# Kernel optimization log

Hardware: AMD Instinct MI355X
Metric: run time of the kernel (lower is better)

Reference implementation:

```python
import jax, jax.numpy as jnp
import numpy as np

B, C, H, W = 8, 512, 32, 32
N_HEADS = 4
D_K = C // N_HEADS  # 128


def setup_inputs() -> dict:
    key = jax.random.key(0)
    k1, k2, k3, k4, k5 = jax.random.split(key, 5)
    x = jax.random.normal(k1, (B, C, H, W), dtype=jnp.float32)
    # projection: Linear(in_ch, n_heads*d_k*3)
    Wp = jax.random.normal(k2, (C, N_HEADS * D_K * 3), dtype=jnp.float32) * (C ** -0.5)
    bp = jax.random.normal(k3, (N_HEADS * D_K * 3,), dtype=jnp.float32) * 0.01
    # output: Linear(n_heads*d_k, in_ch)
    Wo = jax.random.normal(k4, (N_HEADS * D_K, C), dtype=jnp.float32) * ((N_HEADS * D_K) ** -0.5)
    bo = jax.random.normal(k5, (C,), dtype=jnp.float32) * 0.01
    return {"x": x, "Wp": Wp, "bp": bp, "Wo": Wo, "bo": bo}


def reference(x, Wp, bp, Wo, bo):
    b, c, h, w = x.shape
    scale = D_K ** -0.5
    # [B, C, H, W] -> [B, N, C], N = H*W
    xs = x.reshape(b, c, h * w).transpose(0, 2, 1)
    qkv = (xs @ Wp + bp).reshape(b, h * w, N_HEADS, 3 * D_K)
    q, k, v = jnp.split(qkv, 3, axis=-1)  # each [B, N, H, D]
    attn = jnp.einsum('bihd,bjhd->bijh', q, k) * scale
    attn = jax.nn.softmax(attn, axis=2)  # softmax over j (keys)
    out = jnp.einsum('bijh,bjhd->bihd', attn, v)
    out = out.reshape(b, h * w, N_HEADS * D_K)
    out = out @ Wo + bo
    out = out + xs  # residual (note: GroupNorm is unused in the original forward)
    return out.transpose(0, 2, 1).reshape(b, c, h, w)
```

## Files before the change

### kernel.cpp

```cpp
#include <hip/hip_runtime.h>

#define NB 8
#define NC 512
#define NTOK 1024
#define NHEADS 4
#define DKH 128

typedef unsigned short u16;
typedef __attribute__((ext_vector_type(8))) short bf16x8;
typedef __attribute__((ext_vector_type(4))) float f32x4;

__device__ inline u16 f2b(float f) {
    union { float f; unsigned u; } v; v.f = f;
    unsigned r = v.u + 0x7fffu + ((v.u >> 16) & 1u);
    return (u16)(r >> 16);
}

__device__ __forceinline__ void gll16(const u16* g, u16* l) {
    __builtin_amdgcn_global_load_lds((const __attribute__((address_space(1))) unsigned*)g,
                                     (__attribute__((address_space(3))) unsigned*)l, 16, 0, 0);
}

__global__ __launch_bounds__(256) void prep(const float* __restrict__ x, const float* __restrict__ Wp,
                                            const float* __restrict__ Wo,
                                            u16* __restrict__ xsb, u16* __restrict__ WpT, u16* __restrict__ WoT)
{
    __shared__ float tile[32][33];
    const int z = blockIdx.z;
    const float* src; u16* dst; int R, Cc;
    if (z == 0)      { src = Wp; dst = WpT; R = 512; Cc = 1536; }
    else if (z == 1) { if (blockIdx.x >= 16) return; src = Wo; dst = WoT; R = 512; Cc = 512; }
    else             { if (blockIdx.x >= 32) return;
                       src = x + (long)(z-2)*NC*NTOK; dst = xsb + (long)(z-2)*NTOK*NC; R = NC; Cc = NTOK; }
    int c0 = blockIdx.x * 32, r0 = blockIdx.y * 32;
    int tx = threadIdx.x, ty = threadIdx.y;
    #pragma unroll
    for (int k = 0; k < 4; ++k)
        tile[ty + 8*k][tx] = src[(long)(r0 + ty + 8*k) * Cc + c0 + tx];
    __syncthreads();
    #pragma unroll
    for (int k = 0; k < 4; ++k)
        dst[(long)(c0 + ty + 8*k) * R + r0 + tx] = f2b(tile[tx][ty + 8*k]);
}

__global__ __launch_bounds__(512, 2) void gemm_qkv(const u16* __restrict__ WpT, const u16* __restrict__ xsb,
                                                   const float* __restrict__ bp,
                                                   u16* __restrict__ qg, u16* __restrict__ kg, u16* __restrict__ vg)
{
    __shared__ union SmU {
        struct { u16 As[2][256][64]; u16 Bs[2][256][64]; } s;
        u16 Os[8][64][72];
    } sm;
    const int tid = threadIdx.x;
    const int raw = blockIdx.x;
    const int L = (raw & 7) * 24 + (raw >> 3);
    const int mb = L % 6, nb = L / 6;
    const int m0 = mb * 256;
    const int n0 = nb * 256;
    const int w = tid >> 6, lane = tid & 63, quad = lane >> 4, lc = lane & 15;
    const int mo = (w & 1) * 128, no = (w >> 1) * 64;
    const int sw8 = (((lane & 7) ^ (lane >> 3)) << 3);
    const int xs = lc & 7;
    const int srow = (lane >> 3);

    f32x4 acc[8][4] = {};

    #pragma unroll
    for (int p = 0; p < 4; ++p) {
        int row = w*32 + p*8 + srow;
        gll16(&WpT[(long)(m0 + row) * NC + 0 + sw8], &sm.s.As[0][w*32 + p*8][0]);
        gll16(&xsb[(long)(n0 + row) * NC + 0 + sw8], &sm.s.Bs[0][w*32 + p*8][0]);
    }

    for (int t = 0; t < 8; ++t) {
        if (t < 7) {
            const long kk = (long)(t + 1) * 64;
            const int nbuf = (t + 1) & 1;
            #pragma unroll
            for (int p = 0; p < 4; ++p) {
                int row = w*32 + p*8 + srow;
                gll16(&WpT[(long)(m0 + row) * NC + kk + sw8], &sm.s.As[nbuf][w*32 + p*8][0]);
                gll16(&xsb[(long)(n0 + row) * NC + kk + sw8], &sm.s.Bs[nbuf][w*32 + p*8][0]);
            }
            asm volatile("s_waitcnt vmcnt(8)" ::: "memory");
        } else {
            asm volatile("s_waitcnt vmcnt(0)" ::: "memory");
        }
        __builtin_amdgcn_s_barrier();
        __builtin_amdgcn_sched_barrier(0);

        const int cb = t & 1;
        #pragma unroll
        for (int ks = 0; ks < 2; ++ks) {
            bf16x8 af[8], bfr[4];
            #pragma unroll
            for (int mt = 0; mt < 8; ++mt)
                af[mt] = *(const bf16x8*)&sm.s.As[cb][mo + mt*16 + lc][((ks*4 + quad) ^ xs) << 3];
            #pragma unroll
            for (int nt = 0; nt < 4; ++nt)
                bfr[nt] = *(const bf16x8*)&sm.s.Bs[cb][no + nt*16 + lc][((ks*4 + quad) ^ xs) << 3];
            __builtin_amdgcn_s_setprio(1);
            #pragma unroll
            for (int mt = 0; mt < 8; ++mt)
                #pragma unroll
                for (int nt = 0; nt < 4; ++nt)
                    acc[mt][nt] = __builtin_amdgcn_mfma_f32_16x16x32_bf16(af[mt], bfr[nt], acc[mt][nt], 0, 0, 0);
            __builtin_amdgcn_s_setprio(0);
        }
        __builtin_amdgcn_s_barrier();
    }

    const int bb = n0 >> 10;
    const int nblk = n0 & 1023;
    const int pb = (m0 + mo) >> 7;
    const int h = pb / 3;
    const int sel = pb % 3;
    const long bhbase = (long)(bb * NHEADS + h);

    #pragma unroll
    for (int mh = 0; mh < 2; ++mh) {
        const int d0 = mh * 64;
        #pragma unroll
        for (int mt4 = 0; mt4 < 4; ++mt4) {
            int mt = mh*4 + mt4;
            int cq0 = m0 + mo + mt*16 + quad*4;
            float b0 = bp[cq0+0], b1 = bp[cq0+1], b2 = bp[cq0+2], b3 = bp[cq0+3];
            #pragma unroll
            for (int nt = 0; nt < 4; ++nt) {
                f32x4 a = acc[mt][nt];
                int nl = nt*16 + lc;
                int ml = mt4*16 + quad*4;
                u16 e0 = f2b(a[0]+b0), e1 = f2b(a[1]+b1), e2 = f2b(a[2]+b2), e3 = f2b(a[3]+b3);
                if (sel == 2) {
                    sm.Os[w][ml+0][nl] = e0; sm.Os[w][ml+1][nl] = e1;
                    sm.Os[w][ml+2][nl] = e2; sm.Os[w][ml+3][nl] = e3;
                } else {
                    sm.Os[w][nl][ml+0] = e0; sm.Os[w][nl][ml+1] = e1;
                    sm.Os[w][nl][ml+2] = e2; sm.Os[w][nl][ml+3] = e3;
                }
            }
        }
        __builtin_amdgcn_sched_barrier(0);

        if (sel == 2) {
            #pragma unroll
            for (int pass = 0; pass < 8; ++pass) {
                int ml  = pass*8 + srow;
                int nl0 = (lane & 7) * 8;
                bf16x8 vv = *(const bf16x8*)&sm.Os[w][ml][nl0];
                *(bf16x8*)&vg[((bhbase*DKH + d0 + ml) << 10) + nblk + no + sw8] = vv;
            }
        } else if (sel == 1) {
            #pragma unroll
            for (int pass = 0; pass < 8; ++pass) {
                int nl  = pass*8 + srow;
                int ml0 = (lane & 7) * 8;
                bf16x8 vv = *(const bf16x8*)&sm.Os[w][nl][ml0];
                *(bf16x8*)&kg[((bhbase*NTOK + nblk + no + nl) << 7) + d0 + sw8] = vv;
            }
        } else {
            #pragma unroll
            for (int pass = 0; pass < 8; ++pass) {
                int nl  = pass*8 + srow;
                int ml0 = (lane & 7) * 8;
                bf16x8 vv = *(const bf16x8*)&sm.Os[w][nl][ml0];
                *(bf16x8*)&qg[((bhbase*NTOK + nblk + no + nl) << 7) + d0 + ml0] = vv;
            }
        }
        __builtin_amdgcn_sched_barrier(0);
    }
}

__global__ __launch_bounds__(512) void attn(const u16* __restrict__ qg, const u16* __restrict__ kg,
                                            const u16* __restrict__ vtg, u16* __restrict__ ho)
{
    __shared__ union {
        struct { u16 Ks[2][64*128]; u16 Vt[2][128*64]; u16 Ps[8][32][40]; } m;
        struct { float Om[4][2][32][68]; float Lm[2][4][32]; } g;
    } sm;
    const int tid = threadIdx.x;
    const int w = tid >> 6, lane = tid & 63, quad = lane >> 4, lc = lane & 15;
    const int iw = w & 3, jw = w >> 2;
    const int id = blockIdx.x;
    const int xcd = id & 7, rest = id >> 3, sub = rest & 3, bx = rest >> 2;
    const int pr = xcd + sub*8;
    const int b = pr >> 2, h = pr & 3;
    const int i0 = bx*128 + iw*32;
    const long bh = (long)(b * NHEADS + h) << 17;
    const u16* qb = qg + bh;
    const u16* kb = kg + bh;
    const u16* vb = vtg + bh;
    const float SL2E = 0.08838834764831845f * 1.4426950408889634f;

    bf16x8 qf[2][4];
    #pragma unroll
    for (int it = 0; it < 2; ++it)
        #pragma unroll
        for (int ks = 0; ks < 4; ++ks)
            qf[it][ks] = *(const bf16x8*)&qb[(long)(i0 + it*16 + lc) * DKH + ks*32 + quad*8];

    f32x4 o[2][8] = {};
    float lsum[2] = {0.f, 0.f};
    const int xs = lc & 7;

    #pragma unroll
    for (int p = 0; p < 2; ++p) {
        int ck = (w*2 + p)*64 + lane;
        gll16(&kb[(long)ck * 8], &sm.m.Ks[0][(w*2 + p)*512]);
        gll16(&vb[(((long)(ck >> 3)) << 10) + (ck & 7)*8], &sm.m.Vt[0][(w*2 + p)*512]);
    }

    for (int t = 0; t < 16; ++t) {
        __syncthreads();
        if (t < 15) {
            long jo = (long)(t+1) * 64;
            #pragma unroll
            for (int p = 0; p < 2; ++p) {
                int ck = (w*2 + p)*64 + lane;
                gll16(&kb[jo*128 + (long)ck*8], &sm.m.Ks[(t+1)&1][(w*2 + p)*512]);
                gll16(&vb[(((long)(ck >> 3)) << 10) + jo + (ck & 7)*8], &sm.m.Vt[(t+1)&1][(w*2 + p)*512]);
            }
        }
        const u16* K = sm.m.Ks[t&1];
        const u16* V = sm.m.Vt[t&1];

        f32x4 s[2][2] = {};
        #pragma unroll
        for (int ks = 0; ks < 4; ++ks)
            #pragma unroll
            for (int jt = 0; jt < 2; ++jt) {
                bf16x8 kf = *(const bf16x8*)&K[(jw*32 + jt*16 + lc)*128 + (((ks*4 + quad) ^ xs) << 3)];
                s[0][jt] = __builtin_amdgcn_mfma_f32_16x16x32_bf16(kf, qf[0][ks], s[0][jt], 0, 0, 0);
                s[1][jt] = __builtin_amdgcn_mfma_f32_16x16x32_bf16(kf, qf[1][ks], s[1][jt], 0, 0, 0);
            }

        #pragma unroll
        for (int it = 0; it < 2; ++it)
            #pragma unroll
            for (int jt = 0; jt < 2; ++jt) {
                float p0 = __builtin_amdgcn_exp2f(s[it][jt][0] * SL2E);
                float p1 = __builtin_amdgcn_exp2f(s[it][jt][1] * SL2E);
                float p2 = __builtin_amdgcn_exp2f(s[it][jt][2] * SL2E);
                float p3 = __builtin_amdgcn_exp2f(s[it][jt][3] * SL2E);
                lsum[it] += (p0 + p1) + (p2 + p3);
                ushort4 pk;
                pk.x = f2b(p0); pk.y = f2b(p1); pk.z = f2b(p2); pk.w = f2b(p3);
                *(ushort4*)&sm.m.Ps[w][it*16 + lc][jt*16 + quad*4] = pk;
            }
        __builtin_amdgcn_sched_barrier(0);

        bf16x8 pf0 = *(const bf16x8*)&sm.m.Ps[w][lc]     [quad*8];
        bf16x8 pf1 = *(const bf16x8*)&sm.m.Ps[w][16 + lc][quad*8];
        #pragma unroll
        for (int dt = 0; dt < 8; ++dt) {
            bf16x8 vf = *(const bf16x8*)&V[(dt*16 + lc)*64 + (((jw*4 + quad) ^ xs) << 3)];
            o[0][dt] = __builtin_amdgcn_mfma_f32_16x16x32_bf16(vf, pf0, o[0][dt], 0, 0, 0);
            o[1][dt] = __builtin_amdgcn_mfma_f32_16x16x32_bf16(vf, pf1, o[1][dt], 0, 0, 0);
        }
    }

    #pragma unroll
    for (int it = 0; it < 2; ++it) {
        lsum[it] += __shfl_xor(lsum[it], 16);
        lsum[it] += __shfl_xor(lsum[it], 32);
    }

    __syncthreads();
    #pragma unroll
    for (int it = 0; it < 2; ++it) {
        if (jw == 0) {
            #pragma unroll
            for (int d4 = 0; d4 < 4; ++d4)
                *(f32x4*)&sm.g.Om[iw][1][it*16 + lc][d4*16 + quad*4] = o[it][4 + d4];
        } else {
            #pragma unroll
            for (int d4 = 0; d4 < 4; ++d4)
                *(f32x4*)&sm.g.Om[iw][0][it*16 + lc][d4*16 + quad*4] = o[it][d4];
        }
        if (quad == 0) sm.g.Lm[jw][iw][it*16 + lc] = lsum[it];
    }
    __syncthreads();
    #pragma unroll
    for (int it = 0; it < 2; ++it) {
        float lt = lsum[it] + sm.g.Lm[1 - jw][iw][it*16 + lc];
        float inv = 1.0f / lt;
        long rowbase = (long)(b*NTOK + i0 + it*16 + lc) * NC + h*DKH + jw*64;
        if (jw == 0) {
            #pragma unroll
            for (int d4 = 0; d4 < 4; ++d4) {
                f32x4 part = *(const f32x4*)&sm.g.Om[iw][0][it*16 + lc][d4*16 + quad*4];
                f32x4 tot = o[it][d4] + part;
                ushort4 pk;
                pk.x = f2b(tot[0] * inv); pk.y = f2b(tot[1] * inv);
                pk.z = f2b(tot[2] * inv); pk.w = f2b(tot[3] * inv);
                *(ushort4*)&ho[rowbase + d4*16 + quad*4] = pk;
            }
        } else {
            #pragma unroll
            for (int d4 = 0; d4 < 4; ++d4) {
                f32x4 part = *(const f32x4*)&sm.g.Om[iw][1][it*16 + lc][d4*16 + quad*4];
                f32x4 tot = o[it][4 + d4] + part;
                ushort4 pk;
                pk.x = f2b(tot[0] * inv); pk.y = f2b(tot[1] * inv);
                pk.z = f2b(tot[2] * inv); pk.w = f2b(tot[3] * inv);
                *(ushort4*)&ho[rowbase + d4*16 + quad*4] = pk;
            }
        }
    }
}

__global__ __launch_bounds__(256) void gemm_out(const u16* __restrict__ WoT, const u16* __restrict__ ho,
                                                const float* __restrict__ bo, const float* __restrict__ xin,
                                                float* __restrict__ dout)
{
    __shared__ struct { u16 As[128][64]; u16 Bs[64][64]; } sm;
    const int tid = threadIdx.x;
    const int m0 = blockIdx.x * 128;
    const int n0 = blockIdx.y * 64;
    const int w = tid >> 6, lane = tid & 63, quad = lane >> 4, lc = lane & 15;
    const int mo = (w & 1) * 64, no = (w >> 1) * 32;
    const int sw8 = (((lane & 7) ^ (lane >> 3)) << 3);
    const int xs = lc & 7;

    f32x4 acc[4][2] = {};

    for (int k0 = 0; k0 < NC; k0 += 64) {
        __syncthreads();
        #pragma unroll
        for (int p = 0; p < 4; ++p) {
            int row = w*32 + p*8 + (lane >> 3);
            gll16(&WoT[(long)(m0 + row) * NC + k0 + sw8], &sm.As[w*32 + p*8][0]);
        }
        #pragma unroll
        for (int p = 0; p < 2; ++p) {
            int row = w*16 + p*8 + (lane >> 3);
            gll16(&ho[(long)(n0 + row) * NC + k0 + sw8], &sm.Bs[w*16 + p*8][0]);
        }
        __syncthreads();
        #pragma unroll
        for (int ks = 0; ks < 2; ++ks) {
            bf16x8 af[4], bfr[2];
            #pragma unroll
            for (int t = 0; t < 4; ++t)
                af[t] = *(const bf16x8*)&sm.As[mo + t*16 + lc][((ks*4 + quad) ^ xs) << 3];
            #pragma unroll
            for (int t = 0; t < 2; ++t)
                bfr[t] = *(const bf16x8*)&sm.Bs[no + t*16 + lc][((ks*4 + quad) ^ xs) << 3];
            #pragma unroll
            for (int mt = 0; mt < 4; ++mt)
                #pragma unroll
                for (int nt = 0; nt < 2; ++nt)
                    acc[mt][nt] = __builtin_amdgcn_mfma_f32_16x16x32_bf16(af[mt], bfr[nt], acc[mt][nt], 0, 0, 0);
        }
    }

    const int bb = n0 >> 10;
    #pragma unroll
    for (int mt = 0; mt < 4; ++mt) {
        int cc0 = m0 + mo + mt*16 + quad*4;
        float b0 = bo[cc0+0], b1 = bo[cc0+1], b2 = bo[cc0+2], b3 = bo[cc0+3];
        #pragma unroll
        for (int nt = 0; nt < 2; ++nt) {
            int nl = (n0 + no + nt*16 + lc) & (NTOK - 1);
            f32x4 a = acc[mt][nt];
            long ix = ((long)(bb*NC + cc0) << 10) + nl;
            dout[ix]             = a[0] + b0 + xin[ix];
            dout[ix + (1 << 10)] = a[1] + b1 + xin[ix + (1 << 10)];
            dout[ix + (2 << 10)] = a[2] + b2 + xin[ix + (2 << 10)];
            dout[ix + (3 << 10)] = a[3] + b3 + xin[ix + (3 << 10)];
        }
    }
}

extern "C" void kernel_launch(void* const* d_in, const int* in_sizes, int n_in,
                              void* d_out, int out_size, void* d_ws, size_t ws_size,
                              hipStream_t stream)
{
    (void)in_sizes; (void)n_in; (void)out_size; (void)ws_size;
    const float* x  = (const float*)d_in[0];
    const float* Wp = (const float*)d_in[1];
    const float* bp = (const float*)d_in[2];
    const float* Wo = (const float*)d_in[3];
    const float* bo = (const float*)d_in[4];
    float* out = (float*)d_out;

    u16* ws  = (u16*)d_ws;
    u16* xsb = ws;
    u16* WpT = xsb + (long)NB * NTOK * NC;
    u16* WoT = WpT + 1536L * 512;
    u16* qg  = WoT + 512L * 512;
    u16* kg  = qg + (long)NB * NHEADS * NTOK * DKH;
    u16* vtg = kg + (long)NB * NHEADS * NTOK * DKH;
    u16* ho  = vtg + (long)NB * NHEADS * NTOK * DKH;

    prep<<<dim3(48, 16, 10), dim3(32, 8), 0, stream>>>(x, Wp, Wo, xsb, WpT, WoT);
    gemm_qkv<<<dim3(192), 512, 0, stream>>>(WpT, xsb, bp, qg, kg, vtg);
    attn<<<dim3(256), 512, 0, stream>>>(qg, kg, vtg, ho);
    gemm_out<<<dim3(NC/128, (NB*NTOK)/64), 256, 0, stream>>>(WoT, ho, bo, x, out);
}
```

Baseline: 139.3 us.

## Fuse all four stages into one cooperative persistent kernel with grid syncs

Replaces the four separate launches (prep transpose, QKV GEMM, attention, output GEMM) with one cooperative kernel of 256 blocks. Grid-wide syncs separate the stages, and shared memory is a union across stages. The aim is to remove launch gaps and tail effects between kernels. In exchange, the output GEMM and prep work are reshaped to fit a fixed 256-block grid, the QKV stage uses only 192 blocks, and grid.sync adds its own overhead.

```diff
diff --git a/kernel.cpp b/kernel.cpp
--- a/kernel.cpp
+++ b/kernel.cpp
@@ -1,4 +1,7 @@
 #include <hip/hip_runtime.h>
+#include <hip/hip_cooperative_groups.h>
+
+namespace cg = cooperative_groups;
 
 #define NB 8
 #define NC 512
@@ -21,353 +24,345 @@
                                      (__attribute__((address_space(3))) unsigned*)l, 16, 0, 0);
 }
 
-__global__ __launch_bounds__(256) void prep(const float* __restrict__ x, const float* __restrict__ Wp,
-                                            const float* __restrict__ Wo,
-                                            u16* __restrict__ xsb, u16* __restrict__ WpT, u16* __restrict__ WoT)
+__global__ __launch_bounds__(512, 2) void fused(const float* __restrict__ x, const float* __restrict__ Wp,
+                                                const float* __restrict__ bp, const float* __restrict__ Wo,
+                                                const float* __restrict__ bo, float* __restrict__ dout,
+                                                u16* __restrict__ xsb, u16* __restrict__ WpT, u16* __restrict__ WoT,
+                                                u16* __restrict__ qg, u16* __restrict__ kg, u16* __restrict__ vtg,
+                                                u16* __restrict__ ho)
 {
-    __shared__ float tile[32][33];
-    const int z = blockIdx.z;
-    const float* src; u16* dst; int R, Cc;
-    if (z == 0)      { src = Wp; dst = WpT; R = 512; Cc = 1536; }
-    else if (z == 1) { if (blockIdx.x >= 16) return; src = Wo; dst = WoT; R = 512; Cc = 512; }
-    else             { if (blockIdx.x >= 32) return;
-                       src = x + (long)(z-2)*NC*NTOK; dst = xsb + (long)(z-2)*NTOK*NC; R = NC; Cc = NTOK; }
-    int c0 = blockIdx.x * 32, r0 = blockIdx.y * 32;
-    int tx = threadIdx.x, ty = threadIdx.y;
-    #pragma unroll
-    for (int k = 0; k < 4; ++k)
-        tile[ty + 8*k][tx] = src[(long)(r0 + ty + 8*k) * Cc + c0 + tx];
-    __syncthreads();
-    #pragma unroll
-    for (int k = 0; k < 4; ++k)
-        dst[(long)(c0 + ty + 8*k) * R + r0 + tx] = f2b(tile[tx][ty + 8*k]);
-}
-
-__global__ __launch_bounds__(512, 2) void gemm_qkv(const u16* __restrict__ WpT, const u16* __restrict__ xsb,
-                                                   const float* __restrict__ bp,
-                                                   u16* __restrict__ qg, u16* __restrict__ kg, u16* __restrict__ vg)
-{
-    __shared__ union SmU {
-        struct { u16 As[2][256][64]; u16 Bs[2][256][64]; } s;
-        u16 Os[8][64][72];
+    __shared__ union FS {
+        float pt[2][32][33];
+        union { struct { u16 As[2][256][64]; u16 Bs[2][256][64]; } s;
+                u16 Os[8][64][72]; } q;
+        union { struct { u16 Ks[2][8192]; u16 Vt[2][8192]; u16 Ps[8][32][40]; } m;
+                struct { float Om[4][2][32][68]; float Lm[2][4][32]; } g; } a;
+        struct { u16 As[128][64]; u16 Bs[128][64]; } o;
     } sm;
+
+    cg::grid_group grid = cg::this_grid();
     const int tid = threadIdx.x;
-    const int raw = blockIdx.x;
-    const int L = (raw & 7) * 24 + (raw >> 3);
-    const int mb = L % 6, nb = L / 6;
-    const int m0 = mb * 256;
-    const int n0 = nb * 256;
+    const int bid = blockIdx.x;
     const int w = tid >> 6, lane = tid & 63, quad = lane >> 4, lc = lane & 15;
-    const int mo = (w & 1) * 128, no = (w >> 1) * 64;
     const int sw8 = (((lane & 7) ^ (lane >> 3)) << 3);
     const int xs = lc & 7;
-    const int srow = (lane >> 3);
-
-    f32x4 acc[8][4] = {};
-
-    #pragma unroll
-    for (int p = 0; p < 4; ++p) {
-        int row = w*32 + p*8 + srow;
-        gll16(&WpT[(long)(m0 + row) * NC + 0 + sw8], &sm.s.As[0][w*32 + p*8][0]);
-        gll16(&xsb[(long)(n0 + row) * NC + 0 + sw8], &sm.s.Bs[0][w*32 + p*8][0]);
+    const int srow = lane >> 3;
+
+    {
+        const int half = tid >> 8, t256 = tid & 255;
+        const int tx = t256 & 31, ty = t256 >> 5;
+        for (int j = bid*2 + half; j < 5120; j += 512) {
+            const float* src; u16* dst; int R, Cc, bx, by;
+            if (j < 768)       { src = Wp; dst = WpT; R = 512; Cc = 1536; bx = j % 48; by = j / 48; }
+            else if (j < 1024) { int q2 = j - 768; src = Wo; dst = WoT; R = 512; Cc = 512; bx = q2 & 15; by = q2 >> 4; }
+            else               { int q2 = j - 1024; int z = q2 >> 9; int r = q2 & 511;
+                                 src = x + (long)z*NC*NTOK; dst = xsb + (long)z*NTOK*NC;
+                                 R = NC; Cc = NTOK; bx = r & 31; by = r >> 5; }
+            int c0 = bx*32, r0 = by*32;
+            #pragma unroll
+            for (int k = 0; k < 4; ++k)
+                sm.pt[half][ty + 8*k][tx] = src[(long)(r0 + ty + 8*k)*Cc + c0 + tx];
+            __syncthreads();
+            #pragma unroll
+            for (int k = 0; k < 4; ++k)
+                dst[(long)(c0 + ty + 8*k)*R + r0 + tx] = f2b(sm.pt[half][tx][ty + 8*k]);
+            __syncthreads();
+        }
     }
-
-    for (int t = 0; t < 8; ++t) {
-        if (t < 7) {
-            const long kk = (long)(t + 1) * 64;
-            const int nbuf = (t + 1) & 1;
-            #pragma unroll
-            for (int p = 0; p < 4; ++p) {
-                int row = w*32 + p*8 + srow;
-                gll16(&WpT[(long)(m0 + row) * NC + kk + sw8], &sm.s.As[nbuf][w*32 + p*8][0]);
-                gll16(&xsb[(long)(n0 + row) * NC + kk + sw8], &sm.s.Bs[nbuf][w*32 + p*8][0]);
-            }
-            asm volatile("s_waitcnt vmcnt(8)" ::: "memory");
-        } else {
-            asm volatile("s_waitcnt vmcnt(0)" ::: "memory");
-        }
-        __builtin_amdgcn_s_barrier();
-        __builtin_amdgcn_sched_barrier(0);
-
-        const int cb = t & 1;
-        #pragma unroll
-        for (int ks = 0; ks < 2; ++ks) {
-            bf16x8 af[8], bfr[4];
-            #pragma unroll
-            for (int mt = 0; mt < 8; ++mt)
-                af[mt] = *(const bf16x8*)&sm.s.As[cb][mo + mt*16 + lc][((ks*4 + quad) ^ xs) << 3];
-            #pragma unroll
-            for (int nt = 0; nt < 4; ++nt)
-                bfr[nt] = *(const bf16x8*)&sm.s.Bs[cb][no + nt*16 + lc][((ks*4 + quad) ^ xs) << 3];
-            __builtin_amdgcn_s_setprio(1);
-            #pragma unroll
-            for (int mt = 0; mt < 8; ++mt)
+    grid.sync();
+
+    if (bid < 192) {
+        const int L = (bid & 7) * 24 + (bid >> 3);
+        const int mb = L % 6, nb = L / 6;
+        const int m0 = mb * 256, n0 = nb * 256;
+        const int mo = (w & 1) * 128, no = (w >> 1) * 64;
+
+        f32x4 acc[8][4] = {};
+
+        #pragma unroll
+        for (int p = 0; p < 4; ++p) {
+            int row = w*32 + p*8 + srow;
+            gll16(&WpT[(long)(m0 + row) * NC + 0 + sw8], &sm.q.s.As[0][w*32 + p*8][0]);
+            gll16(&xsb[(long)(n0 + row) * NC + 0 + sw8], &sm.q.s.Bs[0][w*32 + p*8][0]);
+        }
+
+        for (int t = 0; t < 8; ++t) {
+            if (t < 7) {
+                const long kk = (long)(t + 1) * 64;
+                const int nbuf = (t + 1) & 1;
+                #pragma unroll
+                for (int p = 0; p < 4; ++p) {
+                    int row = w*32 + p*8 + srow;
+                    gll16(&WpT[(long)(m0 + row) * NC + kk + sw8], &sm.q.s.As[nbuf][w*32 + p*8][0]);
+                    gll16(&xsb[(long)(n0 + row) * NC + kk + sw8], &sm.q.s.Bs[nbuf][w*32 + p*8][0]);
+                }
+                asm volatile("s_waitcnt vmcnt(8)" ::: "memory");
+            } else {
+                asm volatile("s_waitcnt vmcnt(0)" ::: "memory");
+            }
+            __builtin_amdgcn_s_barrier();
+            __builtin_amdgcn_sched_barrier(0);
+
+            const int cb = t & 1;
+            #pragma unroll
+            for (int ks = 0; ks < 2; ++ks) {
+                bf16x8 af[8], bfr[4];
+                #pragma unroll
+                for (int mt = 0; mt < 8; ++mt)
+                    af[mt] = *(const bf16x8*)&sm.q.s.As[cb][mo + mt*16 + lc][((ks*4 + quad) ^ xs) << 3];
                 #pragma unroll
                 for (int nt = 0; nt < 4; ++nt)
-                    acc[mt][nt] = __builtin_amdgcn_mfma_f32_16x16x32_bf16(af[mt], bfr[nt], acc[mt][nt], 0, 0, 0);
-            __builtin_amdgcn_s_setprio(0);
-        }
-        __builtin_amdgcn_s_barrier();
+                    bfr[nt] = *(const bf16x8*)&sm.q.s.Bs[cb][no + nt*16 + lc][((ks*4 + quad) ^ xs) << 3];
+                __builtin_amdgcn_s_setprio(1);
+                #pragma unroll
+                for (int mt = 0; mt < 8; ++mt)
+                    #pragma unroll
+                    for (int nt = 0; nt < 4; ++nt)
+                        acc[mt][nt] = __builtin_amdgcn_mfma_f32_16x16x32_bf16(af[mt], bfr[nt], acc[mt][nt], 0, 0, 0);
+                __builtin_amdgcn_s_setprio(0);
+            }
+            __builtin_amdgcn_s_barrier();
+        }
+
+        const int bb = n0 >> 10;
+        const int nblk = n0 & 1023;
+        const int pb = (m0 + mo) >> 7;
+        const int h = pb / 3;
+        const int sel = pb % 3;
+        const long bhbase = (long)(bb * NHEADS + h);
+
+        #pragma unroll
+        for (int mh = 0; mh < 2; ++mh) {
+            const int d0 = mh * 64;
+            #pragma unroll
+            for (int mt4 = 0; mt4 < 4; ++mt4) {
+                int mt = mh*4 + mt4;
+                int cq0 = m0 + mo + mt*16 + quad*4;
+                float b0 = bp[cq0+0], b1 = bp[cq0+1], b2 = bp[cq0+2], b3 = bp[cq0+3];
+                #pragma unroll
+                for (int nt = 0; nt < 4; ++nt) {
+                    f32x4 aa = acc[mt][nt];
+                    int nl = nt*16 + lc;
+                    int ml = mt4*16 + quad*4;
+                    u16 e0 = f2b(aa[0]+b0), e1 = f2b(aa[1]+b1), e2 = f2b(aa[2]+b2), e3 = f2b(aa[3]+b3);
+                    if (sel == 2) {
+                        sm.q.Os[w][ml+0][nl] = e0; sm.q.Os[w][ml+1][nl] = e1;
+                        sm.q.Os[w][ml+2][nl] = e2; sm.q.Os[w][ml+3][nl] = e3;
+                    } else {
+                        sm.q.Os[w][nl][ml+0] = e0; sm.q.Os[w][nl][ml+1] = e1;
+                        sm.q.Os[w][nl][ml+2] = e2; sm.q.Os[w][nl][ml+3] = e3;
+                    }
+                }
+            }
+            __builtin_amdgcn_sched_barrier(0);
+
+            if (sel == 2) {
+                #pragma unroll
+                for (int pass = 0; pass < 8; ++pass) {
+                    int ml  = pass*8 + srow;
+                    int nl0 = (lane & 7) * 8;
+                    bf16x8 vv = *(const bf16x8*)&sm.q.Os[w][ml][nl0];
+                    *(bf16x8*)&vtg[((bhbase*DKH + d0 + ml) << 10) + nblk + no + sw8] = vv;
+                }
+            } else if (sel == 1) {
+                #pragma unroll
+                for (int pass = 0; pass < 8; ++pass) {
+                    int nl  = pass*8 + srow;
+                    int ml0 = (lane & 7) * 8;
+                    bf16x8 vv = *(const bf16x8*)&sm.q.Os[w][nl][ml0];
+                    *(bf16x8*)&kg[((bhbase*NTOK + nblk + no + nl) << 7) + d0 + sw8] = vv;
+                }
+            } else {
+                #pragma unroll
+                for (int pass = 0; pass < 8; ++pass) {
+                    int nl  = pass*8 + srow;
+                    int ml0 = (lane & 7) * 8;
+                    bf16x8 vv = *(const bf16x8*)&sm.q.Os[w][nl][ml0];
+                    *(bf16x8*)&qg[((bhbase*NTOK + nblk + no + nl) << 7) + d0 + ml0] = vv;
+                }
+            }
+            __builtin_amdgcn_sched_barrier(0);
+        }
     }
-
-    const int bb = n0 >> 10;
-    const int nblk = n0 & 1023;
-    const int pb = (m0 + mo) >> 7;
-    const int h = pb / 3;
-    const int sel = pb % 3;
-    const long bhbase = (long)(bb * NHEADS + h);
-
-    #pragma unroll
-    for (int mh = 0; mh < 2; ++mh) {
-        const int d0 = mh * 64;
-        #pragma unroll
-        for (int mt4 = 0; mt4 < 4; ++mt4) {
-            int mt = mh*4 + mt4;
-            int cq0 = m0 + mo + mt*16 + quad*4;
-            float b0 = bp[cq0+0], b1 = bp[cq0+1], b2 = bp[cq0+2], b3 = bp[cq0+3];
-            #pragma unroll
-            for (int nt = 0; nt < 4; ++nt) {
-                f32x4 a = acc[mt][nt];
-                int nl = nt*16 + lc;
-                int ml = mt4*16 + quad*4;
-                u16 e0 = f2b(a[0]+b0), e1 = f2b(a[1]+b1), e2 = f2b(a[2]+b2), e3 = f2b(a[3]+b3);
-                if (sel == 2) {
-                    sm.Os[w][ml+0][nl] = e0; sm.Os[w][ml+1][nl] = e1;
-                    sm.Os[w][ml+2][nl] = e2; sm.Os[w][ml+3][nl] = e3;
-                } else {
-                    sm.Os[w][nl][ml+0] = e0; sm.Os[w][nl][ml+1] = e1;
-                    sm.Os[w][nl][ml+2] = e2; sm.Os[w][nl][ml+3] = e3;
-                }
-            }
-        }
-        __builtin_amdgcn_sched_barrier(0);
-
-        if (sel == 2) {
-            #pragma unroll
-            for (int pass = 0; pass < 8; ++pass) {
-                int ml  = pass*8 + srow;
-                int nl0 = (lane & 7) * 8;
-                bf16x8 vv = *(const bf16x8*)&sm.Os[w][ml][nl0];
-                *(bf16x8*)&vg[((bhbase*DKH + d0 + ml) << 10) + nblk + no + sw8] = vv;
-            }
-        } else if (sel == 1) {
-            #pragma unroll
-            for (int pass = 0; pass < 8; ++pass) {
-                int nl  = pass*8 + srow;
-                int ml0 = (lane & 7) * 8;
-                bf16x8 vv = *(const bf16x8*)&sm.Os[w][nl][ml0];
-                *(bf16x8*)&kg[((bhbase*NTOK + nblk + no + nl) << 7) + d0 + sw8] = vv;
-            }
-        } else {
-            #pragma unroll
-            for (int pass = 0; pass < 8; ++pass) {
-                int nl  = pass*8 + srow;
-                int ml0 = (lane & 7) * 8;
-                bf16x8 vv = *(const bf16x8*)&sm.Os[w][nl][ml0];
-                *(bf16x8*)&qg[((bhbase*NTOK + nblk + no + nl) << 7) + d0 + ml0] = vv;
-            }
-        }
-        __builtin_amdgcn_sched_barrier(0);
+    grid.sync();
+
+    {
+        const int iw = w & 3, jw = w >> 2;
+        const int xcd = bid & 7, rest = bid >> 3, sub = rest & 3, bx = rest >> 2;
+        const int pr = xcd + sub*8;
+        const int b = pr >> 2, h = pr & 3;
+        const int i0 = bx*128 + iw*32;
+        const long bh = (long)(b * NHEADS + h) << 17;
+        const u16* qb = qg + bh;
+        const u16* kb = kg + bh;
+        const u16* vb = vtg + bh;
+        const float SL2E = 0.08838834764831845f * 1.4426950408889634f;
+
+        bf16x8 qf[2][4];
+        #pragma unroll
+        for (int it = 0; it < 2; ++it)
+            #pragma unroll
+            for (int ks = 0; ks < 4; ++ks)
+                qf[it][ks] = *(const bf16x8*)&qb[(long)(i0 + it*16 + lc) * DKH + ks*32 + quad*8];
+
+        f32x4 o[2][8] = {};
+        float lsum[2] = {0.f, 0.f};
+
+        #pragma unroll
+        for (int p = 0; p < 2; ++p) {
+            int ck = (w*2 + p)*64 + lane;
+            gll16(&kb[(long)ck * 8], &sm.a.m.Ks[0][(w*2 + p)*512]);
+            gll16(&vb[(((long)(ck >> 3)) << 10) + (ck & 7)*8], &sm.a.m.Vt[0][(w*2 + p)*512]);
+        }
+
+        for (int t = 0; t < 16; ++t) {
+            __syncthreads();
+            if (t < 15) {
+                long jo = (long)(t+1) * 64;
+                #pragma unroll
+                for (int p = 0; p < 2; ++p) {
+                    int ck = (w*2 + p)*64 + lane;
+                    gll16(&kb[jo*128 + (long)ck*8], &sm.a.m.Ks[(t+1)&1][(w*2 + p)*512]);
+                    gll16(&vb[(((long)(ck >> 3)) << 10) + jo + (ck & 7)*8], &sm.a.m.Vt[(t+1)&1][(w*2 + p)*512]);
+                }
+            }
+            const u16* K = sm.a.m.Ks[t&1];
+            const u16* V = sm.a.m.Vt[t&1];
+
+            f32x4 s[2][2] = {};
+            #pragma unroll
+            for (int ks = 0; ks < 4; ++ks)
+                #pragma unroll
+                for (int jt = 0; jt < 2; ++jt) {
+                    bf16x8 kf = *(const bf16x8*)&K[(jw*32 + jt*16 + lc)*128 + (((ks*4 + quad) ^ xs) << 3)];
+                    s[0][jt] = __builtin_amdgcn_mfma_f32_16x16x32_bf16(kf, qf[0][ks], s[0][jt], 0, 0, 0);
+                    s[1][jt] = __builtin_amdgcn_mfma_f32_16x16x32_bf16(kf, qf[1][ks], s[1][jt], 0, 0, 0);
+                }
+
+            #pragma unroll
+            for (int it = 0; it < 2; ++it)
+                #pragma unroll
+                for (int jt = 0; jt < 2; ++jt) {
+                    float p0 = __builtin_amdgcn_exp2f(s[it][jt][0] * SL2E);
+                    float p1 = __builtin_amdgcn_exp2f(s[it][jt][1] * SL2E);
+                    float p2 = __builtin_amdgcn_exp2f(s[it][jt][2] * SL2E);
+                    float p3 = __builtin_amdgcn_exp2f(s[it][jt][3] * SL2E);
+                    lsum[it] += (p0 + p1) + (p2 + p3);
+                    ushort4 pk;
+                    pk.x = f2b(p0); pk.y = f2b(p1); pk.z = f2b(p2); pk.w = f2b(p3);
+                    *(ushort4*)&sm.a.m.Ps[w][it*16 + lc][jt*16 + quad*4] = pk;
+                }
+            __builtin_amdgcn_sched_barrier(0);
+
+            bf16x8 pf0 = *(const bf16x8*)&sm.a.m.Ps[w][lc]     [quad*8];
+            bf16x8 pf1 = *(const bf16x8*)&sm.a.m.Ps[w][16 + lc][quad*8];
+            #pragma unroll
+            for (int dt = 0; dt < 8; ++dt) {
+                bf16x8 vf = *(const bf16x8*)&V[(dt*16 + lc)*64 + (((jw*4 + quad) ^ xs) << 3)];
+                o[0][dt] = __builtin_amdgcn_mfma_f32_16x16x32_bf16(vf, pf0, o[0][dt], 0, 0, 0);
+                o[1][dt] = __builtin_amdgcn_mfma_f32_16x16x32_bf16(vf, pf1, o[1][dt], 0, 0, 0);
+            }
+        }
+
+        #pragma unroll
+        for (int it = 0; it < 2; ++it) {
+            lsum[it] += __shfl_xor(lsum[it], 16);
+            lsum[it] += __shfl_xor(lsum[it], 32);
+        }
+
+        __syncthreads();
+        #pragma unroll
+        for (int it = 0; it < 2; ++it) {
+            if (jw == 0) {
+                #pragma unroll
+                for (int d4 = 0; d4 < 4; ++d4)
+                    *(f32x4*)&sm.a.g.Om[iw][1][it*16 + lc][d4*16 + quad*4] = o[it][4 + d4];
+            } else {
+                #pragma unroll
+                for (int d4 = 0; d4 < 4; ++d4)
+                    *(f32x4*)&sm.a.g.Om[iw][0][it*16 + lc][d4*16 + quad*4] = o[it][d4];
+            }
+            if (quad == 0) sm.a.g.Lm[jw][iw][it*16 + lc] = lsum[it];
+        }
+        __syncthreads();
+        #pragma unroll
+        for (int it = 0; it < 2; ++it) {
+            float lt = lsum[it] + sm.a.g.Lm[1 - jw][iw][it*16 + lc];
+            float inv = 1.0f / lt;
+            long rowbase = (long)(b*NTOK + i0 + it*16 + lc) * NC + h*DKH + jw*64;
+            if (jw == 0) {
+                #pragma unroll
+                for (int d4 = 0; d4 < 4; ++d4) {
+                    f32x4 part = *(const f32x4*)&sm.a.g.Om[iw][0][it*16 + lc][d4*16 + quad*4];
+                    f32x4 tot = o[it][d4] + part;
+                    ushort4 pk;
+                    pk.x = f2b(tot[0] * inv); pk.y = f2b(tot[1] * inv);
+                    pk.z = f2b(tot[2] * inv); pk.w = f2b(tot[3] * inv);
+                    *(ushort4*)&ho[rowbase + d4*16 + quad*4] = pk;
+                }
+            } else {
+                #pragma unroll
+                for (int d4 = 0; d4 < 4; ++d4) {
+                    f32x4 part = *(const f32x4*)&sm.a.g.Om[iw][1][it*16 + lc][d4*16 + quad*4];
+                    f32x4 tot = o[it][4 + d4] + part;
+                    ushort4 pk;
+                    pk.x = f2b(tot[0] * inv); pk.y = f2b(tot[1] * inv);
+                    pk.z = f2b(tot[2] * inv); pk.w = f2b(tot[3] * inv);
+                    *(ushort4*)&ho[rowbase + d4*16 + quad*4] = pk;
+                }
+            }
+        }
     }
-}
-
-__global__ __launch_bounds__(512) void attn(const u16* __restrict__ qg, const u16* __restrict__ kg,
-                                            const u16* __restrict__ vtg, u16* __restrict__ ho)
-{
-    __shared__ union {
-        struct { u16 Ks[2][64*128]; u16 Vt[2][128*64]; u16 Ps[8][32][40]; } m;
-        struct { float Om[4][2][32][68]; float Lm[2][4][32]; } g;
-    } sm;
-    const int tid = threadIdx.x;
-    const int w = tid >> 6, lane = tid & 63, quad = lane >> 4, lc = lane & 15;
-    const int iw = w & 3, jw = w >> 2;
-    const int id = blockIdx.x;
-    const int xcd = id & 7, rest = id >> 3, sub = rest & 3, bx = rest >> 2;
-    const int pr = xcd + sub*8;
-    const int b = pr >> 2, h = pr & 3;
-    const int i0 = bx*128 + iw*32;
-    const long bh = (long)(b * NHEADS + h) << 17;
-    const u16* qb = qg + bh;
-    const u16* kb = kg + bh;
-    const u16* vb = vtg + bh;
-    const float SL2E = 0.08838834764831845f * 1.4426950408889634f;
-
-    bf16x8 qf[2][4];
-    #pragma unroll
-    for (int it = 0; it < 2; ++it)
-        #pragma unroll
-        for (int ks = 0; ks < 4; ++ks)
-            qf[it][ks] = *(const bf16x8*)&qb[(long)(i0 + it*16 + lc) * DKH + ks*32 + quad*8];
-
-    f32x4 o[2][8] = {};
-    float lsum[2] = {0.f, 0.f};
-    const int xs = lc & 7;
-
-    #pragma unroll
-    for (int p = 0; p < 2; ++p) {
-        int ck = (w*2 + p)*64 + lane;
-        gll16(&kb[(long)ck * 8], &sm.m.Ks[0][(w*2 + p)*512]);
-        gll16(&vb[(((long)(ck >> 3)) << 10) + (ck & 7)*8], &sm.m.Vt[0][(w*2 + p)*512]);
-    }
-
-    for (int t = 0; t < 16; ++t) {
-        __syncthreads();
-        if (t < 15) {
-            long jo = (long)(t+1) * 64;
+    grid.sync();
+
+    {
+        const int m0 = (bid >> 6) * 128;
+        const int n0 = (bid & 63) * 128;
+        const int mo = (w & 1) * 64, no = (w >> 1) * 32;
+
+        f32x4 acc[4][2] = {};
+
+        for (int k0 = 0; k0 < NC; k0 += 64) {
+            __syncthreads();
             #pragma unroll
             for (int p = 0; p < 2; ++p) {
-                int ck = (w*2 + p)*64 + lane;
-                gll16(&kb[jo*128 + (long)ck*8], &sm.m.Ks[(t+1)&1][(w*2 + p)*512]);
-                gll16(&vb[(((long)(ck >> 3)) << 10) + jo + (ck & 7)*8], &sm.m.Vt[(t+1)&1][(w*2 + p)*512]);
-            }
-        }
-        const u16* K = sm.m.Ks[t&1];
-        const u16* V = sm.m.Vt[t&1];
-
-        f32x4 s[2][2] = {};
-        #pragma unroll
-        for (int ks = 0; ks < 4; ++ks)
-            #pragma unroll
-            for (int jt = 0; jt < 2; ++jt) {
-                bf16x8 kf = *(const bf16x8*)&K[(jw*32 + jt*16 + lc)*128 + (((ks*4 + quad) ^ xs) << 3)];
-                s[0][jt] = __builtin_amdgcn_mfma_f32_16x16x32_bf16(kf, qf[0][ks], s[0][jt], 0, 0, 0);
-                s[1][jt] = __builtin_amdgcn_mfma_f32_16x16x32_bf16(kf, qf[1][ks], s[1][jt], 0, 0, 0);
-            }
-
-        #pragma unroll
-        for (int it = 0; it < 2; ++it)
-            #pragma unroll
-            for (int jt = 0; jt < 2; ++jt) {
-                float p0 = __builtin_amdgcn_exp2f(s[it][jt][0] * SL2E);
-                float p1 = __builtin_amdgcn_exp2f(s[it][jt][1] * SL2E);
-                float p2 = __builtin_amdgcn_exp2f(s[it][jt][2] * SL2E);
-                float p3 = __builtin_amdgcn_exp2f(s[it][jt][3] * SL2E);
-                lsum[it] += (p0 + p1) + (p2 + p3);
-                ushort4 pk;
-                pk.x = f2b(p0); pk.y = f2b(p1); pk.z = f2b(p2); pk.w = f2b(p3);
-                *(ushort4*)&sm.m.Ps[w][it*16 + lc][jt*16 + quad*4] = pk;
-            }
-        __builtin_amdgcn_sched_barrier(0);
-
-        bf16x8 pf0 = *(const bf16x8*)&sm.m.Ps[w][lc]     [quad*8];
-        bf16x8 pf1 = *(const bf16x8*)&sm.m.Ps[w][16 + lc][quad*8];
-        #pragma unroll
-        for (int dt = 0; dt < 8; ++dt) {
-            bf16x8 vf = *(const bf16x8*)&V[(dt*16 + lc)*64 + (((jw*4 + quad) ^ xs) << 3)];
-            o[0][dt] = __builtin_amdgcn_mfma_f32_16x16x32_bf16(vf, pf0, o[0][dt], 0, 0, 0);
-            o[1][dt] = __builtin_amdgcn_mfma_f32_16x16x32_bf16(vf, pf1, o[1][dt], 0, 0, 0);
-        }
-    }
-
-    #pragma unroll
-    for (int it = 0; it < 2; ++it) {
-        lsum[it] += __shfl_xor(lsum[it], 16);
-        lsum[it] += __shfl_xor(lsum[it], 32);
-    }
-
-    __syncthreads();
-    #pragma unroll
-    for (int it = 0; it < 2; ++it) {
-        if (jw == 0) {
-            #pragma unroll
-            for (int d4 = 0; d4 < 4; ++d4)
-                *(f32x4*)&sm.g.Om[iw][1][it*16 + lc][d4*16 + quad*4] = o[it][4 + d4];
-        } else {
-            #pragma unroll
-            for (int d4 = 0; d4 < 4; ++d4)
-                *(f32x4*)&sm.g.Om[iw][0][it*16 + lc][d4*16 + quad*4] = o[it][d4];
-        }
-        if (quad == 0) sm.g.Lm[jw][iw][it*16 + lc] = lsum[it];
-    }
-    __syncthreads();
-    #pragma unroll
-    for (int it = 0; it < 2; ++it) {
-        float lt = lsum[it] + sm.g.Lm[1 - jw][iw][it*16 + lc];
-        float inv = 1.0f / lt;
-        long rowbase = (long)(b*NTOK + i0 + it*16 + lc) * NC + h*DKH + jw*64;
-        if (jw == 0) {
-            #pragma unroll
-            for (int d4 = 0; d4 < 4; ++d4) {
-                f32x4 part = *(const f32x4*)&sm.g.Om[iw][0][it*16 + lc][d4*16 + quad*4];
-                f32x4 tot = o[it][d4] + part;
-                ushort4 pk;
-                pk.x = f2b(tot[0] * inv); pk.y = f2b(tot[1] * inv);
-                pk.z = f2b(tot[2] * inv); pk.w = f2b(tot[3] * inv);
-                *(ushort4*)&ho[rowbase + d4*16 + quad*4] = pk;
-            }
-        } else {
-            #pragma unroll
-            for (int d4 = 0; d4 < 4; ++d4) {
-                f32x4 part = *(const f32x4*)&sm.g.Om[iw][1][it*16 + lc][d4*16 + quad*4];
-                f32x4 tot = o[it][4 + d4] + part;
-                ushort4 pk;
-                pk.x = f2b(tot[0] * inv); pk.y = f2b(tot[1] * inv);
-                pk.z = f2b(tot[2] * inv); pk.w = f2b(tot[3] * inv);
-                *(ushort4*)&ho[rowbase + d4*16 + quad*4] = pk;
-            }
-        }
-    }
-}
-
-__global__ __launch_bounds__(256) void gemm_out(const u16* __restrict__ WoT, const u16* __restrict__ ho,
-                                                const float* __restrict__ bo, const float* __restrict__ xin,
-                                                float* __restrict__ dout)
-{
-    __shared__ struct { u16 As[128][64]; u16 Bs[64][64]; } sm;
-    const int tid = threadIdx.x;
-    const int m0 = blockIdx.x * 128;
-    const int n0 = blockIdx.y * 64;
-    const int w = tid >> 6, lane = tid & 63, quad = lane >> 4, lc = lane & 15;
-    const int mo = (w & 1) * 64, no = (w >> 1) * 32;
-    const int sw8 = (((lane & 7) ^ (lane >> 3)) << 3);
-    const int xs = lc & 7;
-
-    f32x4 acc[4][2] = {};
-
-    for (int k0 = 0; k0 < NC; k0 += 64) {
-        __syncthreads();
-        #pragma unroll
-        for (int p = 0; p < 4; ++p) {
-            int row = w*32 + p*8 + (lane >> 3);
-            gll16(&WoT[(long)(m0 + row) * NC + k0 + sw8], &sm.As[w*32 + p*8][0]);
-        }
-        #pragma unroll
-        for (int p = 0; p < 2; ++p) {
-            int row = w*16 + p*8 + (lane >> 3);
-            gll16(&ho[(long)(n0 + row) * NC + k0 + sw8], &sm.Bs[w*16 + p*8][0]);
-        }
-        __syncthreads();
-        #pragma unroll
-        for (int ks = 0; ks < 2; ++ks) {
-            bf16x8 af[4], bfr[2];
-            #pragma unroll
-            for (int t = 0; t < 4; ++t)
-                af[t] = *(const bf16x8*)&sm.As[mo + t*16 + lc][((ks*4 + quad) ^ xs) << 3];
-            #pragma unroll
-            for (int t = 0; t < 2; ++t)
-                bfr[t] = *(const bf16x8*)&sm.Bs[no + t*16 + lc][((ks*4 + quad) ^ xs) << 3];
-            #pragma unroll
-            for (int mt = 0; mt < 4; ++mt)
-                #pragma unroll
-                for (int nt = 0; nt < 2; ++nt)
-                    acc[mt][nt] = __builtin_amdgcn_mfma_f32_16x16x32_bf16(af[mt], bfr[nt], acc[mt][nt], 0, 0, 0);
-        }
-    }
-
-    const int bb = n0 >> 10;
-    #pragma unroll
-    for (int mt = 0; mt < 4; ++mt) {
-        int cc0 = m0 + mo + mt*16 + quad*4;
-        float b0 = bo[cc0+0], b1 = bo[cc0+1], b2 = bo[cc0+2], b3 = bo[cc0+3];
-        #pragma unroll
-        for (int nt = 0; nt < 2; ++nt) {
-            int nl = (n0 + no + nt*16 + lc) & (NTOK - 1);
-            f32x4 a = acc[mt][nt];
-            long ix = ((long)(bb*NC + cc0) << 10) + nl;
-            dout[ix]             = a[0] + b0 + xin[ix];
-            dout[ix + (1 << 10)] = a[1] + b1 + xin[ix + (1 << 10)];
-            dout[ix + (2 << 10)] = a[2] + b2 + xin[ix + (2 << 10)];
-            dout[ix + (3 << 10)] = a[3] + b3 + xin[ix + (3 << 10)];
+                int row = w*16 + p*8 + srow;
+                gll16(&WoT[(long)(m0 + row) * NC + k0 + sw8], &sm.o.As[w*16 + p*8][0]);
+                gll16(&ho[(long)(n0 + row) * NC + k0 + sw8], &sm.o.Bs[w*16 + p*8][0]);
+            }
+            __syncthreads();
+            #pragma unroll
+            for (int ks = 0; ks < 2; ++ks) {
+                bf16x8 af[4], bfr[2];
+                #pragma unroll
+                for (int t = 0; t < 4; ++t)
+                    af[t] = *(const bf16x8*)&sm.o.As[mo + t*16 + lc][((ks*4 + quad) ^ xs) << 3];
+                #pragma unroll
+                for (int t = 0; t < 2; ++t)
+                    bfr[t] = *(const bf16x8*)&sm.o.Bs[no + t*16 + lc][((ks*4 + quad) ^ xs) << 3];
+                #pragma unroll
+                for (int mt = 0; mt < 4; ++mt)
+                    #pragma unroll
+                    for (int nt = 0; nt < 2; ++nt)
+                        acc[mt][nt] = __builtin_amdgcn_mfma_f32_16x16x32_bf16(af[mt], bfr[nt], acc[mt][nt], 0, 0, 0);
+            }
+        }
+
+        const int bb = n0 >> 10;
+        #pragma unroll
+        for (int mt = 0; mt < 4; ++mt) {
+            int cc0 = m0 + mo + mt*16 + quad*4;
+            float b0 = bo[cc0+0], b1 = bo[cc0+1], b2 = bo[cc0+2], b3 = bo[cc0+3];
+            #pragma unroll
+            for (int nt = 0; nt < 2; ++nt) {
+                int nl = (n0 + no + nt*16 + lc) & (NTOK - 1);
+                f32x4 aa = acc[mt][nt];
+                long ix = ((long)(bb*NC + cc0) << 10) + nl;
+                dout[ix]             = aa[0] + b0 + x[ix];
+                dout[ix + (1 << 10)] = aa[1] + b1 + x[ix + (1 << 10)];
+                dout[ix + (2 << 10)] = aa[2] + b2 + x[ix + (2 << 10)];
+                dout[ix + (3 << 10)] = aa[3] + b3 + x[ix + (3 << 10)];
+            }
         }
     }
 }
@@ -393,8 +388,7 @@
     u16* vtg = kg + (long)NB * NHEADS * NTOK * DKH;
     u16* ho  = vtg + (long)NB * NHEADS * NTOK * DKH;
 
-    prep<<<dim3(48, 16, 10), dim3(32, 8), 0, stream>>>(x, Wp, Wo, xsb, WpT, WoT);
-    gemm_qkv<<<dim3(192), 512, 0, stream>>>(WpT, xsb, bp, qg, kg, vtg);
-    attn<<<dim3(256), 512, 0, stream>>>(qg, kg, vtg, ho);
-    gemm_out<<<dim3(NC/128, (NB*NTOK)/64), 256, 0, stream>>>(WoT, ho, bo, x, out);
+    void* args[] = {(void*)&x, (void*)&Wp, (void*)&bp, (void*)&Wo, (void*)&bo, (void*)&out,
+                    (void*)&xsb, (void*)&WpT, (void*)&WoT, (void*)&qg, (void*)&kg, (void*)&vtg, (void*)&ho};
+    hipLaunchCooperativeKernel((const void*)fused, dim3(256), dim3(512), args, 0, stream);
 }
```

Result: slower. 285.8 us (+105.2%).
